# Optimization experiments

Measured on AMD Instinct MI355X. Metric: run time of the kernel, lower is better.

The kernel has to match this reference:

```python
import jax, jax.numpy as jnp
import numpy as np

GEOM_W = 0.01
N_ITERS = 5
HUBER_DELTA = 1.345
LM_EPS = 1e-6


def _skew(w):
    x, y, z = w[..., 0], w[..., 1], w[..., 2]
    o = jnp.zeros_like(x)
    return jnp.stack([
        jnp.stack([o, -z, y], -1),
        jnp.stack([z, o, -x], -1),
        jnp.stack([-y, x, o], -1)], -2)


def _se3_exp(xi):
    # xi: [B,6] = (v, w), translation first (matches Jt = [I | -skew(X)])
    v, w = xi[..., :3], xi[..., 3:]
    t2 = jnp.sum(w * w, -1)[..., None, None]
    small = t2 < 1e-8
    t2s = jnp.where(small, 1.0, t2)
    th = jnp.sqrt(t2s)
    A = jnp.where(small, 1.0 - t2 / 6.0, jnp.sin(th) / th)
    Bc = jnp.where(small, 0.5 - t2 / 24.0, (1.0 - jnp.cos(th)) / t2s)
    Cc = jnp.where(small, 1.0 / 6.0 - t2 / 120.0, (th - jnp.sin(th)) / (t2s * th))
    wx = _skew(w)
    wx2 = jnp.matmul(wx, wx)
    I3 = jnp.eye(3, dtype=xi.dtype)
    R = I3 + A * wx + Bc * wx2
    V = I3 + Bc * wx + Cc * wx2
    t = jnp.einsum('bij,bj->bi', V, v)
    top = jnp.concatenate([R, t[..., None]], -1)           # [B,3,4]
    bot = jnp.broadcast_to(jnp.array([0.0, 0.0, 0.0, 1.0], dtype=xi.dtype), top[..., :1, :].shape)
    return jnp.concatenate([top, bot], -2)                 # [B,4,4]


def _grid_sample(img, gx, gy):
    # bilinear, padding_mode='zeros', align_corners=True; img [B,C,H,W], gx/gy [B,H,W] in [-1,1]
    B, C, H, W = img.shape
    x = (gx + 1.0) * 0.5 * (W - 1)
    y = (gy + 1.0) * 0.5 * (H - 1)
    x0 = jnp.floor(x)
    y0 = jnp.floor(y)
    fx1 = x - x0
    fy1 = y - y0
    flat = img.reshape(B, C, H * W)

    def corner(xi, yi, wgt):
        inb = (xi >= 0) & (xi <= W - 1) & (yi >= 0) & (yi <= H - 1)
        xc = jnp.clip(xi, 0, W - 1).astype(jnp.int32)
        yc = jnp.clip(yi, 0, H - 1).astype(jnp.int32)
        idx = (yc * W + xc).reshape(B, 1, H * W)
        vals = jnp.take_along_axis(flat, idx, axis=2).reshape(B, C, H, W)
        return vals * (wgt * inb)[:, None]

    return (corner(x0, y0, (1 - fx1) * (1 - fy1)) + corner(x0 + 1, y0, fx1 * (1 - fy1))
            + corner(x0, y0 + 1, (1 - fx1) * fy1) + corner(x0 + 1, y0 + 1, fx1 * fy1))


def _feature_gradient(img):
    # central differences with replicate padding: [B,C,H,W] -> (d/dx, d/dy)
    px = jnp.pad(img, ((0, 0), (0, 0), (0, 0), (1, 1)), mode='edge')
    py = jnp.pad(img, ((0, 0), (0, 0), (1, 1), (0, 0)), mode='edge')
    dx = 0.5 * (px[..., 2:] - px[..., :-2])
    dy = 0.5 * (py[..., 2:, :] - py[..., :-2, :])
    return dx, dy


def _forward(pose, I0, I1, invD0, invD1, intrinsics, depth0, depth1):
    B, C, H, W = I0.shape
    dt = I0.dtype
    fxv = intrinsics[:, 0][:, None, None]
    fyv = intrinsics[:, 1][:, None, None]
    cx = intrinsics[:, 2][:, None, None]
    cy = intrinsics[:, 3][:, None, None]
    vv, uu = jnp.meshgrid(jnp.arange(H, dtype=dt), jnp.arange(W, dtype=dt), indexing='ij')
    d1 = depth1[:, 0]
    # back-projected points in frame 1: [B,H,W,3]
    X1 = jnp.stack([d1 * (uu - cx) / fxv, d1 * (vv - cy) / fyv, d1], -1)
    dI0x, dI0y = _feature_gradient(I0)
    dD0x, dD0y = _feature_gradient(depth0)
    eye3 = jnp.eye(3, dtype=dt)
    lam = GEOM_W
    for _ in range(N_ITERS):
        R = pose[:, :3, :3]
        t = pose[:, :3, 3]
        X0 = jnp.einsum('bij,bhwj->bhwi', R, X1) + t[:, None, None, :]   # [B,H,W,3]
        x, y, z = X0[..., 0], X0[..., 1], X0[..., 2]
        vproj = z > 1e-6
        zs = jnp.where(vproj, z, 1.0)
        u0 = fxv * x / zs + cx
        v0 = fyv * y / zs + cy
        d = z
        inb = (u0 > 0) & (u0 < W - 1) & (v0 > 0) & (v0 < H - 1)
        valid = inb & vproj & (depth0[:, 0] > 0) & (depth1[:, 0] > 0)    # [B,H,W]
        zero = jnp.zeros_like(zs)
        row0 = jnp.stack([fxv / zs + zero, zero, -fxv * x / (zs * zs)], -1)
        row1 = jnp.stack([zero, fyv / zs + zero, -fyv * y / (zs * zs)], -1)
        Jp = jnp.stack([row0, row1], -2)                                  # [B,H,W,2,3]
        Jt = jnp.concatenate([jnp.broadcast_to(eye3, (B, H, W, 3, 3)), -_skew(X0)], -1)  # [B,H,W,3,6]
        Jw = jnp.einsum('bhwij,bhwjk->bhwik', Jp, Jt)                     # [B,H,W,2,6]
        gx = jnp.clip((u0 / (W - 1) - 0.5) * 2.0, -2.0, 2.0)
        gy = jnp.clip((v0 / (H - 1) - 0.5) * 2.0, -2.0, 2.0)
        I0w = _grid_sample(I0, gx, gy)
        r_I = I1 - I0w                                                    # [B,C,H,W]
        D0w = _grid_sample(depth0, gx, gy)
        r_Z = d[:, None] - D0w                                            # [B,1,H,W]
        gI = jnp.stack([_grid_sample(dI0x, gx, gy), _grid_sample(dI0y, gx, gy)], -1)  # [B,C,H,W,2]
        J_I = jnp.einsum('bchwn,bhwnk->bchwk', gI, Jw)                    # [B,C,H,W,6]
        gD = jnp.stack([_grid_sample(dD0x, gx, gy), _grid_sample(dD0y, gx, gy)], -1)  # [B,1,H,W,2]
        J_Z = jnp.einsum('bchwn,bhwnk->bchwk', gD, Jw) - Jt[..., 2, :][:, None]       # [B,1,H,W,6]
        vexp = jnp.broadcast_to(valid[:, None], (B, C + 1, H, W)).reshape(B, -1).astype(dt)
        J = jnp.concatenate([J_I.reshape(B, -1, 6), lam * J_Z.reshape(B, -1, 6)], 1) * vexp[..., None]
        r = jnp.concatenate([r_I.reshape(B, -1), lam * r_Z.reshape(B, -1)], 1) * vexp
        ar = jnp.abs(r)
        wts = jnp.where(ar <= HUBER_DELTA, 1.0, HUBER_DELTA / jnp.maximum(ar, 1e-8))  # Huber M-estimator
        JtJ = jnp.einsum('bnk,bnl->bkl', J, wts[..., None] * J)           # [B,6,6]
        Hs = JtJ + LM_EPS * jnp.eye(6, dtype=dt)                          # LM damping
        Rhs = jnp.einsum('bnk,bn->bk', J, wts * r)                        # [B,6]
        xi = jnp.linalg.solve(Hs, Rhs[..., None])[..., 0]                 # batched 6x6 solve
        pose = jnp.matmul(_se3_exp(xi), pose)                             # left-multiplicative retraction
    return pose


def setup_inputs() -> dict:
    key = jax.random.key(0)
    ks = jax.random.split(key, 5)
    B, C, H, W = 4, 16, 240, 320
    I0 = jax.random.normal(ks[0], (B, C, H, W), jnp.float32)
    I1 = jax.random.normal(ks[1], (B, C, H, W), jnp.float32)
    depth0 = jax.random.uniform(ks[2], (B, 1, H, W), jnp.float32, 0.5, 2.0)
    depth1 = jax.random.uniform(ks[3], (B, 1, H, W), jnp.float32, 0.5, 2.0)
    invD0 = 1.0 / depth0
    invD1 = 1.0 / depth1
    intrinsics = jnp.tile(jnp.array([[250.0, 250.0, (W - 1) / 2.0, (H - 1) / 2.0]], jnp.float32), (B, 1))
    xi0 = 0.01 * jax.random.normal(ks[4], (B, 6), jnp.float32)
    pose = _se3_exp(xi0)
    return {'pose': pose, 'I0': I0, 'I1': I1, 'invD0': invD0, 'invD1': invD1,
            'intrinsics': intrinsics, 'depth0': depth0, 'depth1': depth1}


def reference(pose, I0, I1, invD0, invD1, intrinsics, depth0, depth1):
    return _forward(pose, I0, I1, invD0, invD1, intrinsics, depth0, depth1)
```

## Files before the change

kernel.cpp:

```cpp
#include <hip/hip_runtime.h>
#include <math.h>

#define B_   4
#define C_   16
#define H_   240
#define W_   320
#define HW_  (H_*W_)
#define NBX  128
#define NACC 27
#define GEOM_W_ 0.01f
#define HUBER_  1.345f
#define LM_EPS_ 1e-6
#define N_ITERS_ 5

__global__ void dia_init_pose(const float* __restrict__ pose_in, float* __restrict__ pose) {
    int i = threadIdx.x;
    if (i < B_*16) pose[i] = pose_in[i];
}

__device__ __forceinline__ void samp12(const float* __restrict__ img,
                                       int x0, int y0, int xm1, int xp2, int ym1, int yp2,
                                       float w00, float w10, float w01, float w11,
                                       float& sv, float& sdx, float& sdy)
{
    const float* r0 = img + y0 * W_;
    const float* r1 = r0 + W_;
    float A0 = r0[xm1], A1 = r0[x0], A2 = r0[x0+1], A3 = r0[xp2];
    float B0 = r1[xm1], B1 = r1[x0], B2 = r1[x0+1], B3 = r1[xp2];
    const float* ru = img + ym1 * W_;
    const float* rd = img + yp2 * W_;
    float U0 = ru[x0], U1 = ru[x0+1];
    float D0 = rd[x0], D1 = rd[x0+1];
    sv  = w00*A1 + w10*A2 + w01*B1 + w11*B2;
    sdx = 0.5f*( w00*(A2-A0) + w10*(A3-A1) + w01*(B2-B0) + w11*(B3-B1) );
    sdy = 0.5f*( w00*(B1-U0) + w10*(B2-U1) + w01*(D0-A1) + w11*(D1-A2) );
}

__global__ __launch_bounds__(256) void dia_reduce(
    const float* __restrict__ pose,
    const float* __restrict__ I0,
    const float* __restrict__ I1,
    const float* __restrict__ intr,
    const float* __restrict__ depth0,
    const float* __restrict__ depth1,
    double* __restrict__ partial)
{
    const int b = blockIdx.y;
    const float fxv = intr[b*4+0], fyv = intr[b*4+1];
    const float cx  = intr[b*4+2], cy  = intr[b*4+3];

    float Rm[9], tv[3];
#pragma unroll
    for (int i = 0; i < 3; ++i) {
#pragma unroll
        for (int j = 0; j < 3; ++j) Rm[i*3+j] = pose[b*16 + i*4 + j];
        tv[i] = pose[b*16 + i*4 + 3];
    }

    const float* d0p = depth0 + b * HW_;
    const float* d1p = depth1 + b * HW_;
    const float* I0b = I0 + (size_t)b * C_ * HW_;
    const float* I1b = I1 + (size_t)b * C_ * HW_;

    double acc[NACC];
#pragma unroll
    for (int i = 0; i < NACC; ++i) acc[i] = 0.0;

    for (int p = blockIdx.x * 256 + threadIdx.x; p < HW_; p += NBX * 256) {
        const int v = p / W_;
        const int u = p - v * W_;

        const float d1 = d1p[p];
        const float X1x = d1 * ((float)u - cx) / fxv;
        const float X1y = d1 * ((float)v - cy) / fyv;
        const float X1z = d1;
        const float x = Rm[0]*X1x + Rm[1]*X1y + Rm[2]*X1z + tv[0];
        const float y = Rm[3]*X1x + Rm[4]*X1y + Rm[5]*X1z + tv[1];
        const float z = Rm[6]*X1x + Rm[7]*X1y + Rm[8]*X1z + tv[2];

        const bool vproj = z > 1e-6f;
        const float zs = vproj ? z : 1.0f;
        const float u0 = fxv * x / zs + cx;
        const float v0 = fyv * y / zs + cy;
        const bool inb = (u0 > 0.f) && (u0 < (float)(W_-1)) && (v0 > 0.f) && (v0 < (float)(H_-1));
        const bool valid = inb && vproj && (d0p[p] > 0.f) && (d1 > 0.f);
        if (!valid) continue;

        const float x0f = floorf(u0), y0f = floorf(v0);
        const int x0 = (int)x0f, y0 = (int)y0f;
        const float fx1 = u0 - x0f, fy1 = v0 - y0f;
        const float w00 = (1.f-fx1)*(1.f-fy1), w10 = fx1*(1.f-fy1);
        const float w01 = (1.f-fx1)*fy1,       w11 = fx1*fy1;
        const int xm1 = max(x0-1, 0), xp2 = min(x0+2, W_-1);
        const int ym1 = max(y0-1, 0), yp2 = min(y0+2, H_-1);

        const float iz = 1.f / zs;
        float Jp[2][3];
        Jp[0][0] = fxv * iz; Jp[0][1] = 0.f;       Jp[0][2] = -fxv * x * iz * iz;
        Jp[1][0] = 0.f;      Jp[1][1] = fyv * iz;  Jp[1][2] = -fyv * y * iz * iz;
        float Jt2[3][6] = {
            {1.f, 0.f, 0.f, 0.f,  z,  -y},
            {0.f, 1.f, 0.f, -z,  0.f,  x},
            {0.f, 0.f, 1.f,  y,  -x,  0.f}
        };
        float Jw[2][6];
#pragma unroll
        for (int i = 0; i < 2; ++i)
#pragma unroll
            for (int j = 0; j < 6; ++j)
                Jw[i][j] = Jp[i][0]*Jt2[0][j] + Jp[i][1]*Jt2[1][j] + Jp[i][2]*Jt2[2][j];

        float D0w, dDx, dDy;
        samp12(d0p, x0, y0, xm1, xp2, ym1, yp2, w00, w10, w01, w11, D0w, dDx, dDy);
        const float rZ = z - D0w;
        float JZ[6];
#pragma unroll
        for (int j = 0; j < 6; ++j) JZ[j] = dDx*Jw[0][j] + dDy*Jw[1][j] - Jt2[2][j];
        const float arz = fabsf(GEOM_W_ * rZ);
        const float wz = (arz <= HUBER_) ? 1.f : HUBER_ / fmaxf(arz, 1e-8f);
        const float wz2 = wz * GEOM_W_ * GEOM_W_;

        float Ga = 0.f, Gb = 0.f, Gd = 0.f, grx = 0.f, gry = 0.f;
#pragma unroll 4
        for (int c = 0; c < C_; ++c) {
            const float* ip = I0b + c * HW_;
            float Iw, gxc, gyc;
            samp12(ip, x0, y0, xm1, xp2, ym1, yp2, w00, w10, w01, w11, Iw, gxc, gyc);
            const float r = I1b[c * HW_ + p] - Iw;
            const float ar = fabsf(r);
            const float wc = (ar <= HUBER_) ? 1.f : HUBER_ / fmaxf(ar, 1e-8f);
            Ga  += wc * gxc * gxc;
            Gb  += wc * gxc * gyc;
            Gd  += wc * gyc * gyc;
            grx += wc * r * gxc;
            gry += wc * r * gyc;
        }

        int k = 0;
#pragma unroll
        for (int i = 0; i < 6; ++i) {
#pragma unroll
            for (int j = i; j < 6; ++j) {
                const float vterm = Ga * Jw[0][i] * Jw[0][j]
                                  + Gb * (Jw[0][i] * Jw[1][j] + Jw[1][i] * Jw[0][j])
                                  + Gd * Jw[1][i] * Jw[1][j]
                                  + wz2 * JZ[i] * JZ[j];
                acc[k++] += (double)vterm;
            }
        }
#pragma unroll
        for (int i = 0; i < 6; ++i)
            acc[21 + i] += (double)(grx * Jw[0][i] + gry * Jw[1][i] + wz2 * rZ * JZ[i]);
    }

    __shared__ double sred[4][NACC];
    const int lane = threadIdx.x & 63;
    const int wid  = threadIdx.x >> 6;
#pragma unroll
    for (int i = 0; i < NACC; ++i) {
        double vsum = acc[i];
#pragma unroll
        for (int off = 32; off > 0; off >>= 1) vsum += __shfl_down(vsum, off, 64);
        if (lane == 0) sred[wid][i] = vsum;
    }
    __syncthreads();
    if (threadIdx.x < NACC) {
        double s = sred[0][threadIdx.x] + sred[1][threadIdx.x]
                 + sred[2][threadIdx.x] + sred[3][threadIdx.x];
        partial[((size_t)blockIdx.x * B_ + b) * NACC + threadIdx.x] = s;
    }
}

__global__ __launch_bounds__(128) void dia_solve(const double* __restrict__ partial,
                                                 float* __restrict__ pose)
{
    __shared__ double S[B_][NACC];
    const int t = threadIdx.x;
    if (t < B_ * NACC) {
        const int b = t / NACC, i = t - b * NACC;
        double s = 0.0;
        for (int k = 0; k < NBX; ++k) s += partial[((size_t)k * B_ + b) * NACC + i];
        S[b][i] = s;
    }
    __syncthreads();
    if (t < B_) {
        double Hm[6][7];
        {
            double JtJ[6][6];
            int k = 0;
            for (int i = 0; i < 6; ++i)
                for (int j = i; j < 6; ++j) { JtJ[i][j] = S[t][k]; JtJ[j][i] = S[t][k]; ++k; }
            for (int i = 0; i < 6; ++i) {
                for (int j = 0; j < 6; ++j) Hm[i][j] = JtJ[i][j] + (i == j ? LM_EPS_ : 0.0);
                Hm[i][6] = S[t][21 + i];
            }
        }
        double xi[6];
        for (int col = 0; col < 6; ++col) {
            int piv = col; double mx = fabs(Hm[col][col]);
            for (int r2 = col+1; r2 < 6; ++r2) { double a = fabs(Hm[r2][col]); if (a > mx) { mx = a; piv = r2; } }
            if (piv != col)
                for (int j2 = col; j2 < 7; ++j2) { double tmp = Hm[col][j2]; Hm[col][j2] = Hm[piv][j2]; Hm[piv][j2] = tmp; }
            const double inv = 1.0 / Hm[col][col];
            for (int r2 = col+1; r2 < 6; ++r2) {
                const double f = Hm[r2][col] * inv;
                for (int j2 = col; j2 < 7; ++j2) Hm[r2][j2] -= f * Hm[col][j2];
            }
        }
        for (int r2 = 5; r2 >= 0; --r2) {
            double s = Hm[r2][6];
            for (int j2 = r2+1; j2 < 6; ++j2) s -= Hm[r2][j2] * xi[j2];
            xi[r2] = s / Hm[r2][r2];
        }

        const double vx = xi[0], vy = xi[1], vz = xi[2];
        const double wx = xi[3], wy = xi[4], wz = xi[5];
        const double t2 = wx*wx + wy*wy + wz*wz;
        double A, Bc, Cc;
        if (t2 < 1e-8) {
            A  = 1.0 - t2 / 6.0;
            Bc = 0.5 - t2 / 24.0;
            Cc = 1.0/6.0 - t2 / 120.0;
        } else {
            const double th = sqrt(t2);
            const double sth = sin(th), cth = cos(th);
            A  = sth / th;
            Bc = (1.0 - cth) / t2;
            Cc = (th - sth) / (t2 * th);
        }
        const double Wm[9]  = { 0.0, -wz,  wy,
                                wz,  0.0, -wx,
                               -wy,  wx,  0.0 };
        double W2[9];
        for (int i = 0; i < 3; ++i)
            for (int j = 0; j < 3; ++j) {
                double s = 0.0;
                for (int k = 0; k < 3; ++k) s += Wm[i*3+k] * Wm[k*3+j];
                W2[i*3+j] = s;
            }
        double Rm[9], Vm[9];
        for (int i = 0; i < 9; ++i) {
            const double id = (i % 4 == 0) ? 1.0 : 0.0;
            Rm[i] = id + A  * Wm[i] + Bc * W2[i];
            Vm[i] = id + Bc * Wm[i] + Cc * W2[i];
        }
        const double tx = Vm[0]*vx + Vm[1]*vy + Vm[2]*vz;
        const double ty = Vm[3]*vx + Vm[4]*vy + Vm[5]*vz;
        const double tz = Vm[6]*vx + Vm[7]*vy + Vm[8]*vz;

        float* P = pose + t * 16;
        double Pm[16];
        for (int i = 0; i < 16; ++i) Pm[i] = (double)P[i];
        double E[16] = { Rm[0], Rm[1], Rm[2], tx,
                         Rm[3], Rm[4], Rm[5], ty,
                         Rm[6], Rm[7], Rm[8], tz,
                         0.0,   0.0,   0.0,   1.0 };
        double out[16];
        for (int i = 0; i < 4; ++i)
            for (int j = 0; j < 4; ++j) {
                double s = 0.0;
                for (int k = 0; k < 4; ++k) s += E[i*4+k] * Pm[k*4+j];
                out[i*4+j] = s;
            }
        for (int i = 0; i < 16; ++i) P[i] = (float)out[i];
    }
}

extern "C" void kernel_launch(void* const* d_in, const int* in_sizes, int n_in,
                              void* d_out, int out_size, void* d_ws, size_t ws_size,
                              hipStream_t stream) {
    const float* pose_in = (const float*)d_in[0];
    const float* I0      = (const float*)d_in[1];
    const float* I1      = (const float*)d_in[2];
    const float* intr    = (const float*)d_in[5];
    const float* depth0  = (const float*)d_in[6];
    const float* depth1  = (const float*)d_in[7];

    float*  pose    = (float*)d_out;
    double* partial = (double*)d_ws;

    hipLaunchKernelGGL(dia_init_pose, dim3(1), dim3(64), 0, stream, pose_in, pose);
    for (int it = 0; it < N_ITERS_; ++it) {
        hipLaunchKernelGGL(dia_reduce, dim3(NBX, B_), dim3(256), 0, stream,
                           pose, I0, I1, intr, depth0, depth1, partial);
        hipLaunchKernelGGL(dia_solve, dim3(1), dim3(128), 0, stream, partial, pose);
    }
}
```

Baseline: 394.5 us.

## Split channels across half-blocks, one pixel per thread, atomic double accumulation

The reduce kernel now gives each thread exactly one pixel, with the two halves of a 256-thread block each handling 8 of the 16 channels, and launches many more blocks (HW/128 per batch). Per-thread accumulation and wave reductions move from double to float, and block sums are added to a per-iteration global double buffer with atomics, so the solve kernel no longer loops over partials. Divisions are replaced by reciprocal multiplies and the warp Jacobian is written out in closed form. This is meant to raise occupancy and memory-level parallelism and to avoid slow FP64 shuffles. The cost is float partial sums, many atomics, nondeterministic summation order, and a zeroing step in the init kernel.

```diff
diff --git a/kernel.cpp b/kernel.cpp
--- a/kernel.cpp
+++ b/kernel.cpp
@@ -6,16 +6,19 @@
 #define H_   240
 #define W_   320
 #define HW_  (H_*W_)
-#define NBX  128
+#define NPB  128
+#define NBLK (HW_/NPB)
 #define NACC 27
 #define GEOM_W_ 0.01f
 #define HUBER_  1.345f
 #define LM_EPS_ 1e-6
 #define N_ITERS_ 5
 
-__global__ void dia_init_pose(const float* __restrict__ pose_in, float* __restrict__ pose) {
-    int i = threadIdx.x;
-    if (i < B_*16) pose[i] = pose_in[i];
+__global__ void dia_init(const float* __restrict__ pose_in, float* __restrict__ pose,
+                         double* __restrict__ acc) {
+    const int i = threadIdx.x;
+    if (i < N_ITERS_ * B_ * NACC) acc[i] = 0.0;
+    if (i < B_ * 16) pose[i] = pose_in[i];
 }
 
 __device__ __forceinline__ void samp12(const float* __restrict__ img,
@@ -36,18 +39,23 @@
     sdy = 0.5f*( w00*(B1-U0) + w10*(B2-U1) + w01*(D0-A1) + w11*(D1-A2) );
 }
 
-__global__ __launch_bounds__(256) void dia_reduce(
+__global__ __launch_bounds__(256, 6) void dia_reduce(
     const float* __restrict__ pose,
     const float* __restrict__ I0,
     const float* __restrict__ I1,
     const float* __restrict__ intr,
     const float* __restrict__ depth0,
     const float* __restrict__ depth1,
-    double* __restrict__ partial)
+    double* __restrict__ acc)
 {
-    const int b = blockIdx.y;
+    const int b    = blockIdx.y;
+    const int half = threadIdx.x >> 7;
+    const int lp   = threadIdx.x & 127;
+    const int p    = blockIdx.x * NPB + lp;
+
     const float fxv = intr[b*4+0], fyv = intr[b*4+1];
     const float cx  = intr[b*4+2], cy  = intr[b*4+3];
+    const float ifx = 1.0f / fxv,  ify = 1.0f / fyv;
 
     float Rm[9], tv[3];
 #pragma unroll
@@ -59,128 +67,129 @@
 
     const float* d0p = depth0 + b * HW_;
     const float* d1p = depth1 + b * HW_;
-    const float* I0b = I0 + (size_t)b * C_ * HW_;
-    const float* I1b = I1 + (size_t)b * C_ * HW_;
-
-    double acc[NACC];
-#pragma unroll
-    for (int i = 0; i < NACC; ++i) acc[i] = 0.0;
-
-    for (int p = blockIdx.x * 256 + threadIdx.x; p < HW_; p += NBX * 256) {
+    const float* I0b = I0 + (size_t)b * C_ * HW_ + (size_t)(half * 8) * HW_;
+    const float* I1b = I1 + (size_t)b * C_ * HW_ + (size_t)(half * 8) * HW_;
+
+    float c27[NACC];
+#pragma unroll
+    for (int i = 0; i < NACC; ++i) c27[i] = 0.f;
+
+    {
         const int v = p / W_;
         const int u = p - v * W_;
 
         const float d1 = d1p[p];
-        const float X1x = d1 * ((float)u - cx) / fxv;
-        const float X1y = d1 * ((float)v - cy) / fyv;
-        const float X1z = d1;
-        const float x = Rm[0]*X1x + Rm[1]*X1y + Rm[2]*X1z + tv[0];
-        const float y = Rm[3]*X1x + Rm[4]*X1y + Rm[5]*X1z + tv[1];
-        const float z = Rm[6]*X1x + Rm[7]*X1y + Rm[8]*X1z + tv[2];
+        const float d0 = d0p[p];
+        const float X1x = d1 * ((float)u - cx) * ifx;
+        const float X1y = d1 * ((float)v - cy) * ify;
+        const float x = Rm[0]*X1x + Rm[1]*X1y + Rm[2]*d1 + tv[0];
+        const float y = Rm[3]*X1x + Rm[4]*X1y + Rm[5]*d1 + tv[1];
+        const float z = Rm[6]*X1x + Rm[7]*X1y + Rm[8]*d1 + tv[2];
 
         const bool vproj = z > 1e-6f;
         const float zs = vproj ? z : 1.0f;
-        const float u0 = fxv * x / zs + cx;
-        const float v0 = fyv * y / zs + cy;
+        const float iz = 1.0f / zs;
+        const float u0 = fxv * x * iz + cx;
+        const float v0 = fyv * y * iz + cy;
         const bool inb = (u0 > 0.f) && (u0 < (float)(W_-1)) && (v0 > 0.f) && (v0 < (float)(H_-1));
-        const bool valid = inb && vproj && (d0p[p] > 0.f) && (d1 > 0.f);
-        if (!valid) continue;
-
-        const float x0f = floorf(u0), y0f = floorf(v0);
-        const int x0 = (int)x0f, y0 = (int)y0f;
-        const float fx1 = u0 - x0f, fy1 = v0 - y0f;
-        const float w00 = (1.f-fx1)*(1.f-fy1), w10 = fx1*(1.f-fy1);
-        const float w01 = (1.f-fx1)*fy1,       w11 = fx1*fy1;
-        const int xm1 = max(x0-1, 0), xp2 = min(x0+2, W_-1);
-        const int ym1 = max(y0-1, 0), yp2 = min(y0+2, H_-1);
-
-        const float iz = 1.f / zs;
-        float Jp[2][3];
-        Jp[0][0] = fxv * iz; Jp[0][1] = 0.f;       Jp[0][2] = -fxv * x * iz * iz;
-        Jp[1][0] = 0.f;      Jp[1][1] = fyv * iz;  Jp[1][2] = -fyv * y * iz * iz;
-        float Jt2[3][6] = {
-            {1.f, 0.f, 0.f, 0.f,  z,  -y},
-            {0.f, 1.f, 0.f, -z,  0.f,  x},
-            {0.f, 0.f, 1.f,  y,  -x,  0.f}
-        };
-        float Jw[2][6];
-#pragma unroll
-        for (int i = 0; i < 2; ++i)
-#pragma unroll
-            for (int j = 0; j < 6; ++j)
-                Jw[i][j] = Jp[i][0]*Jt2[0][j] + Jp[i][1]*Jt2[1][j] + Jp[i][2]*Jt2[2][j];
-
-        float D0w, dDx, dDy;
-        samp12(d0p, x0, y0, xm1, xp2, ym1, yp2, w00, w10, w01, w11, D0w, dDx, dDy);
-        const float rZ = z - D0w;
-        float JZ[6];
-#pragma unroll
-        for (int j = 0; j < 6; ++j) JZ[j] = dDx*Jw[0][j] + dDy*Jw[1][j] - Jt2[2][j];
-        const float arz = fabsf(GEOM_W_ * rZ);
-        const float wz = (arz <= HUBER_) ? 1.f : HUBER_ / fmaxf(arz, 1e-8f);
-        const float wz2 = wz * GEOM_W_ * GEOM_W_;
-
-        float Ga = 0.f, Gb = 0.f, Gd = 0.f, grx = 0.f, gry = 0.f;
-#pragma unroll 4
-        for (int c = 0; c < C_; ++c) {
-            const float* ip = I0b + c * HW_;
-            float Iw, gxc, gyc;
-            samp12(ip, x0, y0, xm1, xp2, ym1, yp2, w00, w10, w01, w11, Iw, gxc, gyc);
-            const float r = I1b[c * HW_ + p] - Iw;
-            const float ar = fabsf(r);
-            const float wc = (ar <= HUBER_) ? 1.f : HUBER_ / fmaxf(ar, 1e-8f);
-            Ga  += wc * gxc * gxc;
-            Gb  += wc * gxc * gyc;
-            Gd  += wc * gyc * gyc;
-            grx += wc * r * gxc;
-            gry += wc * r * gyc;
-        }
-
-        int k = 0;
-#pragma unroll
-        for (int i = 0; i < 6; ++i) {
-#pragma unroll
-            for (int j = i; j < 6; ++j) {
-                const float vterm = Ga * Jw[0][i] * Jw[0][j]
-                                  + Gb * (Jw[0][i] * Jw[1][j] + Jw[1][i] * Jw[0][j])
-                                  + Gd * Jw[1][i] * Jw[1][j]
-                                  + wz2 * JZ[i] * JZ[j];
-                acc[k++] += (double)vterm;
-            }
-        }
-#pragma unroll
-        for (int i = 0; i < 6; ++i)
-            acc[21 + i] += (double)(grx * Jw[0][i] + gry * Jw[1][i] + wz2 * rZ * JZ[i]);
-    }
-
-    __shared__ double sred[4][NACC];
+        const bool valid = inb && vproj && (d0 > 0.f) && (d1 > 0.f);
+
+        if (valid) {
+            const float x0f = floorf(u0), y0f = floorf(v0);
+            const int x0 = (int)x0f, y0 = (int)y0f;
+            const float fx1 = u0 - x0f, fy1 = v0 - y0f;
+            const float w00 = (1.f-fx1)*(1.f-fy1), w10 = fx1*(1.f-fy1);
+            const float w01 = (1.f-fx1)*fy1,       w11 = fx1*fy1;
+            const int xm1 = max(x0-1, 0), xp2 = min(x0+2, W_-1);
+            const int ym1 = max(y0-1, 0), yp2 = min(y0+2, H_-1);
+
+            float Jw[2][6];
+            {
+                const float a0 = fxv * iz;
+                const float a2 = -fxv * x * iz * iz;
+                const float b1 = fyv * iz;
+                const float b2 = -fyv * y * iz * iz;
+                Jw[0][0] = a0;        Jw[0][1] = 0.f;      Jw[0][2] = a2;
+                Jw[0][3] = a2 * y;    Jw[0][4] = a0*z - a2*x; Jw[0][5] = -a0*y;
+                Jw[1][0] = 0.f;       Jw[1][1] = b1;       Jw[1][2] = b2;
+                Jw[1][3] = -b1*z + b2*y; Jw[1][4] = -b2*x; Jw[1][5] = b1*x;
+            }
+
+            float JZ[6] = {0.f,0.f,0.f,0.f,0.f,0.f};
+            float wz2 = 0.f, rZ = 0.f;
+            if (half == 0) {
+                float D0w, dDx, dDy;
+                samp12(d0p, x0, y0, xm1, xp2, ym1, yp2, w00, w10, w01, w11, D0w, dDx, dDy);
+                rZ = z - D0w;
+                JZ[0] = dDx*Jw[0][0] + dDy*Jw[1][0];
+                JZ[1] = dDx*Jw[0][1] + dDy*Jw[1][1];
+                JZ[2] = dDx*Jw[0][2] + dDy*Jw[1][2] - 1.f;
+                JZ[3] = dDx*Jw[0][3] + dDy*Jw[1][3] - y;
+                JZ[4] = dDx*Jw[0][4] + dDy*Jw[1][4] + x;
+                JZ[5] = dDx*Jw[0][5] + dDy*Jw[1][5];
+                const float arz = fabsf(GEOM_W_ * rZ);
+                const float wzw = (arz <= HUBER_) ? 1.f : HUBER_ / fmaxf(arz, 1e-8f);
+                wz2 = wzw * GEOM_W_ * GEOM_W_;
+            }
+
+            float Ga = 0.f, Gb = 0.f, Gd = 0.f, grx = 0.f, gry = 0.f;
+            for (int c = 0; c < 8; ++c) {
+                const float* ip = I0b + c * HW_;
+                float Iw, gxc, gyc;
+                samp12(ip, x0, y0, xm1, xp2, ym1, yp2, w00, w10, w01, w11, Iw, gxc, gyc);
+                const float r = I1b[c * HW_ + p] - Iw;
+                const float ar = fabsf(r);
+                const float wc = (ar <= HUBER_) ? 1.f : HUBER_ / fmaxf(ar, 1e-8f);
+                Ga  += wc * gxc * gxc;
+                Gb  += wc * gxc * gyc;
+                Gd  += wc * gyc * gyc;
+                grx += wc * r * gxc;
+                gry += wc * r * gyc;
+            }
+
+            int k = 0;
+#pragma unroll
+            for (int i = 0; i < 6; ++i) {
+#pragma unroll
+                for (int j = i; j < 6; ++j) {
+                    c27[k++] = Ga * Jw[0][i] * Jw[0][j]
+                             + Gb * (Jw[0][i] * Jw[1][j] + Jw[1][i] * Jw[0][j])
+                             + Gd * Jw[1][i] * Jw[1][j]
+                             + wz2 * JZ[i] * JZ[j];
+                }
+            }
+#pragma unroll
+            for (int i = 0; i < 6; ++i)
+                c27[21 + i] = grx * Jw[0][i] + gry * Jw[1][i] + wz2 * rZ * JZ[i];
+        }
+    }
+
+    __shared__ float sred[4][NACC];
     const int lane = threadIdx.x & 63;
     const int wid  = threadIdx.x >> 6;
 #pragma unroll
     for (int i = 0; i < NACC; ++i) {
-        double vsum = acc[i];
-#pragma unroll
-        for (int off = 32; off > 0; off >>= 1) vsum += __shfl_down(vsum, off, 64);
-        if (lane == 0) sred[wid][i] = vsum;
+        float vs = c27[i];
+#pragma unroll
+        for (int off = 32; off > 0; off >>= 1) vs += __shfl_down(vs, off, 64);
+        if (lane == 0) sred[wid][i] = vs;
     }
     __syncthreads();
     if (threadIdx.x < NACC) {
-        double s = sred[0][threadIdx.x] + sred[1][threadIdx.x]
-                 + sred[2][threadIdx.x] + sred[3][threadIdx.x];
-        partial[((size_t)blockIdx.x * B_ + b) * NACC + threadIdx.x] = s;
-    }
-}
-
-__global__ __launch_bounds__(128) void dia_solve(const double* __restrict__ partial,
+        const double s = (double)sred[0][threadIdx.x] + (double)sred[1][threadIdx.x]
+                       + (double)sred[2][threadIdx.x] + (double)sred[3][threadIdx.x];
+        atomicAdd(&acc[b * NACC + threadIdx.x], s);
+    }
+}
+
+__global__ __launch_bounds__(128) void dia_solve(const double* __restrict__ acc,
                                                  float* __restrict__ pose)
 {
     __shared__ double S[B_][NACC];
     const int t = threadIdx.x;
     if (t < B_ * NACC) {
         const int b = t / NACC, i = t - b * NACC;
-        double s = 0.0;
-        for (int k = 0; k < NBX; ++k) s += partial[((size_t)k * B_ + b) * NACC + i];
-        S[b][i] = s;
+        S[b][i] = acc[b * NACC + i];
     }
     __syncthreads();
     if (t < B_) {
@@ -276,13 +285,14 @@
     const float* depth0  = (const float*)d_in[6];
     const float* depth1  = (const float*)d_in[7];
 
-    float*  pose    = (float*)d_out;
-    double* partial = (double*)d_ws;
-
-    hipLaunchKernelGGL(dia_init_pose, dim3(1), dim3(64), 0, stream, pose_in, pose);
+    float*  pose = (float*)d_out;
+    double* acc  = (double*)d_ws;
+
+    hipLaunchKernelGGL(dia_init, dim3(1), dim3(576), 0, stream, pose_in, pose, acc);
     for (int it = 0; it < N_ITERS_; ++it) {
-        hipLaunchKernelGGL(dia_reduce, dim3(NBX, B_), dim3(256), 0, stream,
-                           pose, I0, I1, intr, depth0, depth1, partial);
-        hipLaunchKernelGGL(dia_solve, dim3(1), dim3(128), 0, stream, partial, pose);
-    }
-}
+        double* acc_it = acc + (size_t)it * B_ * NACC;
+        hipLaunchKernelGGL(dia_reduce, dim3(NBLK, B_), dim3(256), 0, stream,
+                           pose, I0, I1, intr, depth0, depth1, acc_it);
+        hipLaunchKernelGGL(dia_solve, dim3(1), dim3(128), 0, stream, acc_it, pose);
+    }
+}
```

New measurement: 451.6 us. +14.5%, slower.
